# Kernel tuning notes

Hardware: AMD Instinct MI355X
Metric: run time of the kernel (lower is better)

## Reference

```python
import jax, jax.numpy as jnp
import numpy as np

N = 100000   # n_nodes
E = 600000   # n_edges
D = 128      # cfg_node_encoding_dim
L = 4        # nr_layers
EPS = 1e-5


def setup_inputs() -> dict:
    key = jax.random.key(0)
    k0, k1, k2, k3 = jax.random.split(key, 4)
    x = jax.random.normal(k0, (N, D), dtype=jnp.float32)
    edge_index = jax.random.randint(k1, (2, E), 0, N, dtype=jnp.int32)
    W = jax.random.normal(k2, (L, D, D), dtype=jnp.float32) * (1.0 / np.sqrt(D))
    b = jax.random.normal(k3, (L, D), dtype=jnp.float32) * 0.01
    gamma = jnp.ones((L, D), dtype=jnp.float32)
    beta = jnp.zeros((L, D), dtype=jnp.float32)
    return {"x": x, "W": W, "b": b, "gamma": gamma, "beta": beta,
            "edge_index": edge_index}


def _gcn_layer(x, W, b, src_sl, dst_sl, norm):
    # PyG GCNConv: h = x @ W, then symmetric-normalized aggregation + bias
    h = x @ W                                  # [N, D]
    msg = h[src_sl] * norm[:, None]            # [E+N, D] gather + scale
    out = jax.ops.segment_sum(msg, dst_sl, num_segments=N)  # scatter-add
    return out + b


def _layer_norm(x, gamma, beta):
    mu = jnp.mean(x, axis=-1, keepdims=True)
    var = jnp.mean(jnp.square(x - mu), axis=-1, keepdims=True)
    return (x - mu) * jax.lax.rsqrt(var + EPS) * gamma + beta


def reference(x, W, b, gamma, beta, edge_index):
    src, dst = edge_index[0], edge_index[1]
    loops = jnp.arange(N, dtype=edge_index.dtype)
    src_sl = jnp.concatenate([src, loops])     # add_self_loops=True
    dst_sl = jnp.concatenate([dst, loops])
    deg = jax.ops.segment_sum(jnp.ones(E + N, dtype=x.dtype), dst_sl,
                              num_segments=N)
    dinv = jnp.where(deg > 0, jax.lax.rsqrt(deg), 0.0)
    norm = dinv[src_sl] * dinv[dst_sl]         # D^{-1/2} (A+I) D^{-1/2}
    h = x
    for i in range(L):
        h = _gcn_layer(h, W[i], b[i], src_sl, dst_sl, norm)
        h = jax.nn.relu(h)
        # dropout is identity in eval mode
        h = _layer_norm(h, gamma[i], beta[i])
    return h
```

## Files before the change

kernel.cpp:

```cpp
#include <hip/hip_runtime.h>
#include <hip/hip_bf16.h>

#define D_DIM 128
#define AST 136

typedef __attribute__((ext_vector_type(8))) short short8v;
typedef __attribute__((ext_vector_type(4))) short short4v;
typedef __attribute__((ext_vector_type(4))) float floatx4;

__device__ __forceinline__ short f2bf(float x) {
    unsigned u = __builtin_bit_cast(unsigned, x);
    unsigned r = u + 0x7fff + ((u >> 16) & 1);
    return (short)(r >> 16);
}
__device__ __forceinline__ float bflo(unsigned p) {
    return __builtin_bit_cast(float, p << 16);
}
__device__ __forceinline__ float bfhi(unsigned p) {
    return __builtin_bit_cast(float, p & 0xffff0000u);
}


__global__ void zero_cnt_kernel(int* __restrict__ cnt, int n) {
    int i = blockIdx.x * blockDim.x + threadIdx.x;
    if (i < n) cnt[i] = 0;
}

__global__ void count_kernel(const int* __restrict__ dst, int* __restrict__ cnt, int e) {
    int i = blockIdx.x * blockDim.x + threadIdx.x;
    if (i < e) atomicAdd(&cnt[dst[i]], 1);
}

__global__ __launch_bounds__(256) void partial_kernel(const int* __restrict__ cnt,
                                                      int* __restrict__ partial, int n) {
    const int b = blockIdx.x, t = threadIdx.x;
    const int base = b * 1024 + t * 4;
    int s = 0;
    if (base + 3 < n) {
        int4 c = *(const int4*)(cnt + base);
        s = c.x + c.y + c.z + c.w;
    } else {
        for (int j = 0; j < 4; ++j) if (base + j < n) s += cnt[base + j];
    }
    #pragma unroll
    for (int m = 1; m < 64; m <<= 1) s += __shfl_xor(s, m, 64);
    __shared__ int ws[4];
    if ((t & 63) == 0) ws[t >> 6] = s;
    __syncthreads();
    if (t == 0) partial[b] = ws[0] + ws[1] + ws[2] + ws[3];
}

__global__ __launch_bounds__(1024) void scan_partials_kernel(int* __restrict__ partial, int nb,
                                                             int* __restrict__ row_ptr,
                                                             int n, int e) {
    __shared__ int sh[1024];
    const int t = threadIdx.x;
    sh[t] = (t < nb) ? partial[t] : 0;
    __syncthreads();
    for (int off = 1; off < 1024; off <<= 1) {
        int v = (t >= off) ? sh[t - off] : 0;
        __syncthreads();
        sh[t] += v;
        __syncthreads();
    }
    if (t < nb) partial[t] = (t == 0) ? 0 : sh[t - 1];
    if (t == 0) row_ptr[n] = e;
}

__global__ __launch_bounds__(256) void emit_kernel(const int* __restrict__ cnt,
                                                   const int* __restrict__ partial,
                                                   int* __restrict__ row_ptr,
                                                   int* __restrict__ cursor,
                                                   float* __restrict__ dinv, int n) {
    const int b = blockIdx.x, t = threadIdx.x;
    const int base = b * 1024 + t * 4;
    int4 c = make_int4(0, 0, 0, 0);
    if (base + 3 < n) {
        c = *(const int4*)(cnt + base);
    } else {
        if (base     < n) c.x = cnt[base];
        if (base + 1 < n) c.y = cnt[base + 1];
        if (base + 2 < n) c.z = cnt[base + 2];
        if (base + 3 < n) c.w = cnt[base + 3];
    }
    const int ts = c.x + c.y + c.z + c.w;
    int incl = ts;
    const int lane = t & 63;
    #pragma unroll
    for (int off = 1; off < 64; off <<= 1) {
        int v = __shfl_up(incl, off, 64);
        if (lane >= off) incl += v;
    }
    __shared__ int wsum[4];
    if (lane == 63) wsum[t >> 6] = incl;
    __syncthreads();
    const int w = t >> 6;
    int waveoff = 0;
    #pragma unroll
    for (int i = 0; i < 3; ++i) if (i < w) waveoff += wsum[i];
    const int basev = partial[b] + waveoff + (incl - ts);
    const int e0 = basev, e1 = e0 + c.x, e2 = e1 + c.y, e3 = e2 + c.z;
    if (base + 3 < n) {
        *(int4*)(row_ptr + base) = make_int4(e0, e1, e2, e3);
        *(int4*)(cursor  + base) = make_int4(e0, e1, e2, e3);
        *(float4*)(dinv + base) = make_float4(rsqrtf((float)(c.x + 1)), rsqrtf((float)(c.y + 1)),
                                              rsqrtf((float)(c.z + 1)), rsqrtf((float)(c.w + 1)));
    } else {
        int es[4] = {e0, e1, e2, e3};
        int cs[4] = {c.x, c.y, c.z, c.w};
        for (int j = 0; j < 4; ++j) if (base + j < n) {
            row_ptr[base + j] = es[j];
            cursor[base + j]  = es[j];
            dinv[base + j]    = rsqrtf((float)(cs[j] + 1));
        }
    }
}

__global__ void fill_kernel(const int* __restrict__ src, const int* __restrict__ dst,
                            const float* __restrict__ dinv,
                            int* __restrict__ cursor, int2* __restrict__ meta, int e) {
    int i = blockIdx.x * blockDim.x + threadIdx.x;
    if (i < e) {
        int s = src[i], d = dst[i];
        int p = atomicAdd(&cursor[d], 1);
        float w = dinv[s] * dinv[d];
        meta[p] = make_int2(s, __builtin_bit_cast(int, w));
    }
}

__global__ __launch_bounds__(256) void wt_prep_kernel(const float* __restrict__ W,
                                                      short* __restrict__ Wt, int total) {
    int o = blockIdx.x * blockDim.x + threadIdx.x;
    if (o >= total) return;
    int l = o >> 14;
    int r = o & 16383;
    int nn = r >> 7;
    int k  = r & 127;
    Wt[o] = f2bf(W[(size_t)l * 16384 + (size_t)k * 128 + nn]);
}

template <bool IN_F32>
__global__ __launch_bounds__(256) void gemm_mfma_kernel(const void* __restrict__ Xv,
                                                        const short* __restrict__ Wt,
                                                        short* __restrict__ H, int n) {
    __shared__ short Alds[64 * AST];
    const int t    = threadIdx.x;
    const int wv   = t >> 6;
    const int lane = t & 63;
    const int m    = lane & 15;
    const int quad = lane >> 4;
    const int row0 = blockIdx.x * 64;

    short8v bfr[2][4];
    #pragma unroll
    for (int c = 0; c < 2; ++c) {
        const short* bp = Wt + (size_t)((wv * 2 + c) * 16 + m) * D_DIM + quad * 8;
        #pragma unroll
        for (int kt = 0; kt < 4; ++kt)
            bfr[c][kt] = *(const short8v*)(bp + kt * 32);
    }

    if constexpr (IN_F32) {
        const float* X = (const float*)Xv;
        #pragma unroll
        for (int i = 0; i < 8; ++i) {
            int q  = t + i * 256;
            int r  = q >> 5;
            int k4 = q & 31;
            int row = row0 + r;
            float4 v = make_float4(0.f, 0.f, 0.f, 0.f);
            if (row < n) v = *(const float4*)(X + (size_t)row * D_DIM + k4 * 4);
            short4v s;
            s.x = f2bf(v.x); s.y = f2bf(v.y); s.z = f2bf(v.z); s.w = f2bf(v.w);
            *(short4v*)(&Alds[r * AST + k4 * 4]) = s;
        }
    } else {
        const short* X = (const short*)Xv;
        #pragma unroll
        for (int i = 0; i < 4; ++i) {
            int q  = t + i * 256;
            int r  = q >> 4;
            int kc = q & 15;
            int row = row0 + r;
            short8v v = {0,0,0,0,0,0,0,0};
            if (row < n) v = *(const short8v*)(X + (size_t)row * D_DIM + kc * 8);
            *(short8v*)(&Alds[r * AST + kc * 8]) = v;
        }
    }
    __syncthreads();

    #pragma unroll
    for (int rt = 0; rt < 4; ++rt) {
        const short* ab = &Alds[(rt * 16 + m) * AST + quad * 8];
        short8v afr[4];
        #pragma unroll
        for (int kt = 0; kt < 4; ++kt) afr[kt] = *(const short8v*)(ab + kt * 32);

        #pragma unroll
        for (int c = 0; c < 2; ++c) {
            floatx4 acc = (floatx4){0.f, 0.f, 0.f, 0.f};
            #pragma unroll
            for (int kt = 0; kt < 4; ++kt)
                acc = __builtin_amdgcn_mfma_f32_16x16x32_bf16(afr[kt], bfr[c][kt], acc, 0, 0, 0);
            const int col = (wv * 2 + c) * 16 + m;
            #pragma unroll
            for (int r = 0; r < 4; ++r) {
                const int row = row0 + rt * 16 + quad * 4 + r;
                if (row < n) H[(size_t)row * D_DIM + col] = f2bf(acc[r]);
            }
        }
    }
}

template <bool OUT_BF16>
__global__ __launch_bounds__(256) void agg_kernel(const short* __restrict__ Hb,
                                                  const int* __restrict__ row_ptr,
                                                  const int2* __restrict__ meta,
                                                  const float* __restrict__ dinv,
                                                  const float* __restrict__ bias,
                                                  const float* __restrict__ gamma,
                                                  const float* __restrict__ beta,
                                                  void* __restrict__ Yv, int n) {
    const int wave = __builtin_amdgcn_readfirstlane(threadIdx.x >> 6);
    const int lane = threadIdx.x & 63;
    const int v = blockIdx.x * 4 + wave;
    if (v >= n) return;

    const float dv = dinv[v];
    const int beg = row_ptr[v];
    const int end = row_ptr[v + 1];

    const unsigned ps = ((const unsigned*)(Hb + (size_t)v * D_DIM))[lane];
    const float wself = dv * dv;
    float ax = bflo(ps) * wself;
    float ay = bfhi(ps) * wself;

    for (int i = beg; i < end; i += 8) {
        int   idx[8];
        float wgt[8];
        #pragma unroll
        for (int j = 0; j < 8; ++j) {
            const int ii = min(i + j, end - 1);
            const int2 mm = meta[ii];
            idx[j] = mm.x;
            wgt[j] = (i + j < end) ? __builtin_bit_cast(float, mm.y) : 0.f;
        }
        unsigned p[8];
        #pragma unroll
        for (int j = 0; j < 8; ++j)
            p[j] = ((const unsigned*)(Hb + (size_t)idx[j] * D_DIM))[lane];
        #pragma unroll
        for (int j = 0; j < 8; ++j) {
            ax = fmaf(wgt[j], bflo(p[j]), ax);
            ay = fmaf(wgt[j], bfhi(p[j]), ay);
        }
    }

    const float2 bb = ((const float2*)bias)[lane];
    float a0 = fmaxf(ax + bb.x, 0.f);
    float a1 = fmaxf(ay + bb.y, 0.f);

    float s1 = a0 + a1;
    float s2 = a0 * a0 + a1 * a1;
    #pragma unroll
    for (int m = 1; m < 64; m <<= 1) {
        s1 += __shfl_xor(s1, m, 64);
        s2 += __shfl_xor(s2, m, 64);
    }
    const float mu  = s1 * (1.f / 128.f);
    const float var = s2 * (1.f / 128.f) - mu * mu;
    const float rs  = rsqrtf(var + 1e-5f);

    const float2 gg = ((const float2*)gamma)[lane];
    const float2 be = ((const float2*)beta)[lane];
    const float o0 = (a0 - mu) * rs * gg.x + be.x;
    const float o1 = (a1 - mu) * rs * gg.y + be.y;

    if constexpr (OUT_BF16) {
        unsigned pack = (unsigned)(unsigned short)f2bf(o0) |
                        ((unsigned)(unsigned short)f2bf(o1) << 16);
        ((unsigned*)((short*)Yv + (size_t)v * D_DIM))[lane] = pack;
    } else {
        float2 o; o.x = o0; o.y = o1;
        ((float2*)((float*)Yv + (size_t)v * D_DIM))[lane] = o;
    }
}


extern "C" void kernel_launch(void* const* d_in, const int* in_sizes, int n_in,
                              void* d_out, int out_size, void* d_ws, size_t ws_size,
                              hipStream_t stream) {
    const float* x     = (const float*)d_in[0];
    const float* W     = (const float*)d_in[1];
    const float* bias  = (const float*)d_in[2];
    const float* gamma = (const float*)d_in[3];
    const float* beta  = (const float*)d_in[4];
    const int*   edges = (const int*)d_in[5];

    const int N = in_sizes[0] / D_DIM;
    const int E = in_sizes[5] / 2;
    const int L = in_sizes[1] / (D_DIM * D_DIM);

    const int* src = edges;
    const int* dst = edges + E;

    const int NB = (N + 1023) / 1024;

    char* w = (char*)d_ws;
    short* Hb   = (short*)w; w += (size_t)N * D_DIM * sizeof(short);
    short* Act  = (short*)w; w += (size_t)N * D_DIM * sizeof(short);
    int* cnt     = (int*)w;  w += (size_t)((N + 3) & ~3) * sizeof(int);
    int* row_ptr = (int*)w;  w += (size_t)((N + 4) & ~3) * sizeof(int);
    int* cursor  = (int*)w;  w += (size_t)((N + 3) & ~3) * sizeof(int);
    int2* meta   = (int2*)w; w += (size_t)E * sizeof(int2);
    float* dinv  = (float*)w; w += (size_t)((N + 3) & ~3) * sizeof(float);
    int* partial = (int*)w;  w += (size_t)((NB + 3) & ~3) * sizeof(int);
    short* Wt    = (short*)w; w += (size_t)L * D_DIM * D_DIM * sizeof(short);

    zero_cnt_kernel<<<(N + 255) / 256, 256, 0, stream>>>(cnt, N);
    count_kernel<<<(E + 255) / 256, 256, 0, stream>>>(dst, cnt, E);
    partial_kernel<<<NB, 256, 0, stream>>>(cnt, partial, N);
    scan_partials_kernel<<<1, 1024, 0, stream>>>(partial, NB, row_ptr, N, E);
    emit_kernel<<<NB, 256, 0, stream>>>(cnt, partial, row_ptr, cursor, dinv, N);
    fill_kernel<<<(E + 255) / 256, 256, 0, stream>>>(src, dst, dinv, cursor, meta, E);

    const int WT_TOTAL = L * D_DIM * D_DIM;
    wt_prep_kernel<<<(WT_TOTAL + 255) / 256, 256, 0, stream>>>(W, Wt, WT_TOTAL);

    const int GB = (N + 63) / 64;
    const int AB = (N + 3) / 4;

    gemm_mfma_kernel<true><<<GB, 256, 0, stream>>>(x, Wt, Hb, N);
    agg_kernel<true><<<AB, 256, 0, stream>>>(Hb, row_ptr, meta, dinv,
                                             bias, gamma, beta, Act, N);
    for (int l = 1; l < L - 1; ++l) {
        gemm_mfma_kernel<false><<<GB, 256, 0, stream>>>(Act, Wt + (size_t)l * D_DIM * D_DIM, Hb, N);
        agg_kernel<true><<<AB, 256, 0, stream>>>(Hb, row_ptr, meta, dinv,
                                                 bias + (size_t)l * D_DIM,
                                                 gamma + (size_t)l * D_DIM,
                                                 beta + (size_t)l * D_DIM, Act, N);
    }
    {
        int l = L - 1;
        gemm_mfma_kernel<false><<<GB, 256, 0, stream>>>(Act, Wt + (size_t)l * D_DIM * D_DIM, Hb, N);
        agg_kernel<false><<<AB, 256, 0, stream>>>(Hb, row_ptr, meta, dinv,
                                                  bias + (size_t)l * D_DIM,
                                                  gamma + (size_t)l * D_DIM,
                                                  beta + (size_t)l * D_DIM, d_out, N);
    }
}
```

Before: 381.8 us.

## Fuse aggregation, GEMM, bias, ReLU and LayerNorm into one per-layer kernel

Reorders each GCN layer to aggregate first and transform second, (A·X)·W instead of A·(X·W). Each block of 64 rows gathers the normalized neighbor sum into LDS as bf16, runs the MFMA GEMM, and applies bias, ReLU and LayerNorm in-register, using LDS atomics for the row statistics. This removes the separate GEMM output buffer and its round trip through global memory, and halves the launches per layer. In exchange, the first layer gathers fp32 input rows, outputs are written as per-column scalar stores, and the aggregation runs serially over 16 rows per wave inside the block.

```diff
diff --git a/kernel.cpp b/kernel.cpp
--- a/kernel.cpp
+++ b/kernel.cpp
@@ -139,11 +139,21 @@
     Wt[o] = f2bf(W[(size_t)l * 16384 + (size_t)k * 128 + nn]);
 }
 
-template <bool IN_F32>
-__global__ __launch_bounds__(256) void gemm_mfma_kernel(const void* __restrict__ Xv,
-                                                        const short* __restrict__ Wt,
-                                                        short* __restrict__ H, int n) {
+template <bool IN_F32, bool OUT_F32>
+__global__ __launch_bounds__(256, 4) void fused_layer_kernel(const void* __restrict__ Xv,
+                                                             const short* __restrict__ Wt,
+                                                             const int* __restrict__ row_ptr,
+                                                             const int2* __restrict__ meta,
+                                                             const float* __restrict__ dinv,
+                                                             const float* __restrict__ bias,
+                                                             const float* __restrict__ gamma,
+                                                             const float* __restrict__ beta,
+                                                             void* __restrict__ Yv, int n) {
     __shared__ short Alds[64 * AST];
+    __shared__ float Ps1[64 * 17];
+    __shared__ float Ps2[64 * 17];
+    __shared__ float2 MuRs[64];
+
     const int t    = threadIdx.x;
     const int wv   = t >> 6;
     const int lane = t & 63;
@@ -151,6 +161,8 @@
     const int quad = lane >> 4;
     const int row0 = blockIdx.x * 64;
 
+    for (int i = t; i < 64 * 17; i += 256) { Ps1[i] = 0.f; Ps2[i] = 0.f; }
+
     short8v bfr[2][4];
     #pragma unroll
     for (int c = 0; c < 2; ++c) {
@@ -160,129 +172,137 @@
             bfr[c][kt] = *(const short8v*)(bp + kt * 32);
     }
 
-    if constexpr (IN_F32) {
-        const float* X = (const float*)Xv;
-        #pragma unroll
-        for (int i = 0; i < 8; ++i) {
-            int q  = t + i * 256;
-            int r  = q >> 5;
-            int k4 = q & 31;
-            int row = row0 + r;
-            float4 v = make_float4(0.f, 0.f, 0.f, 0.f);
-            if (row < n) v = *(const float4*)(X + (size_t)row * D_DIM + k4 * 4);
-            short4v s;
-            s.x = f2bf(v.x); s.y = f2bf(v.y); s.z = f2bf(v.z); s.w = f2bf(v.w);
-            *(short4v*)(&Alds[r * AST + k4 * 4]) = s;
-        }
-    } else {
-        const short* X = (const short*)Xv;
-        #pragma unroll
-        for (int i = 0; i < 4; ++i) {
-            int q  = t + i * 256;
-            int r  = q >> 4;
-            int kc = q & 15;
-            int row = row0 + r;
-            short8v v = {0,0,0,0,0,0,0,0};
-            if (row < n) v = *(const short8v*)(X + (size_t)row * D_DIM + kc * 8);
-            *(short8v*)(&Alds[r * AST + kc * 8]) = v;
-        }
-    }
-    __syncthreads();
-
+    for (int rr = 0; rr < 16; ++rr) {
+        const int v = row0 + wv * 16 + rr;
+        float ax = 0.f, ay = 0.f;
+        if (v < n) {
+            const float dv = dinv[v];
+            const int beg = row_ptr[v];
+            const int end = row_ptr[v + 1];
+            const float wself = dv * dv;
+            if constexpr (IN_F32) {
+                const float2 p = ((const float2*)((const float*)Xv + (size_t)v * D_DIM))[lane];
+                ax = p.x * wself; ay = p.y * wself;
+            } else {
+                const unsigned p = ((const unsigned*)((const short*)Xv + (size_t)v * D_DIM))[lane];
+                ax = bflo(p) * wself; ay = bfhi(p) * wself;
+            }
+            for (int i = beg; i < end; i += 8) {
+                int   idx[8];
+                float wgt[8];
+                #pragma unroll
+                for (int j = 0; j < 8; ++j) {
+                    const int ii = min(i + j, end - 1);
+                    const int2 mm = meta[ii];
+                    idx[j] = mm.x;
+                    wgt[j] = (i + j < end) ? __builtin_bit_cast(float, mm.y) : 0.f;
+                }
+                if constexpr (IN_F32) {
+                    float2 p[8];
+                    #pragma unroll
+                    for (int j = 0; j < 8; ++j)
+                        p[j] = ((const float2*)((const float*)Xv + (size_t)idx[j] * D_DIM))[lane];
+                    #pragma unroll
+                    for (int j = 0; j < 8; ++j) {
+                        ax = fmaf(wgt[j], p[j].x, ax);
+                        ay = fmaf(wgt[j], p[j].y, ay);
+                    }
+                } else {
+                    unsigned p[8];
+                    #pragma unroll
+                    for (int j = 0; j < 8; ++j)
+                        p[j] = ((const unsigned*)((const short*)Xv + (size_t)idx[j] * D_DIM))[lane];
+                    #pragma unroll
+                    for (int j = 0; j < 8; ++j) {
+                        ax = fmaf(wgt[j], bflo(p[j]), ax);
+                        ay = fmaf(wgt[j], bfhi(p[j]), ay);
+                    }
+                }
+            }
+        }
+        const unsigned pk = (unsigned)(unsigned short)f2bf(ax) |
+                            ((unsigned)(unsigned short)f2bf(ay) << 16);
+        *(unsigned*)&Alds[(wv * 16 + rr) * AST + lane * 2] = pk;
+    }
+    __syncthreads();
+
+    floatx4 acc[4][2];
     #pragma unroll
     for (int rt = 0; rt < 4; ++rt) {
         const short* ab = &Alds[(rt * 16 + m) * AST + quad * 8];
         short8v afr[4];
         #pragma unroll
         for (int kt = 0; kt < 4; ++kt) afr[kt] = *(const short8v*)(ab + kt * 32);
-
         #pragma unroll
         for (int c = 0; c < 2; ++c) {
-            floatx4 acc = (floatx4){0.f, 0.f, 0.f, 0.f};
+            floatx4 a = (floatx4){0.f, 0.f, 0.f, 0.f};
             #pragma unroll
             for (int kt = 0; kt < 4; ++kt)
-                acc = __builtin_amdgcn_mfma_f32_16x16x32_bf16(afr[kt], bfr[c][kt], acc, 0, 0, 0);
-            const int col = (wv * 2 + c) * 16 + m;
-            #pragma unroll
-            for (int r = 0; r < 4; ++r) {
-                const int row = row0 + rt * 16 + quad * 4 + r;
-                if (row < n) H[(size_t)row * D_DIM + col] = f2bf(acc[r]);
+                a = __builtin_amdgcn_mfma_f32_16x16x32_bf16(afr[kt], bfr[c][kt], a, 0, 0, 0);
+            acc[rt][c] = a;
+        }
+    }
+
+    const int col0 = wv * 32 + m;
+    const int col1 = col0 + 16;
+    const float b0 = bias[col0], b1 = bias[col1];
+    #pragma unroll
+    for (int rt = 0; rt < 4; ++rt) {
+        #pragma unroll
+        for (int r = 0; r < 4; ++r) {
+            const float v0 = fmaxf(acc[rt][0][r] + b0, 0.f);
+            const float v1 = fmaxf(acc[rt][1][r] + b1, 0.f);
+            acc[rt][0][r] = v0;
+            acc[rt][1][r] = v1;
+            const int row = rt * 16 + quad * 4 + r;
+            atomicAdd(&Ps1[row * 17 + m], v0 + v1);
+            atomicAdd(&Ps2[row * 17 + m], v0 * v0 + v1 * v1);
+        }
+    }
+    __syncthreads();
+
+    {
+        const int row = t >> 2;
+        const int g = t & 3;
+        float s1 = 0.f, s2 = 0.f;
+        #pragma unroll
+        for (int j = 0; j < 4; ++j) {
+            s1 += Ps1[row * 17 + g * 4 + j];
+            s2 += Ps2[row * 17 + g * 4 + j];
+        }
+        s1 += __shfl_xor(s1, 1, 64);  s2 += __shfl_xor(s2, 1, 64);
+        s1 += __shfl_xor(s1, 2, 64);  s2 += __shfl_xor(s2, 2, 64);
+        if (g == 0) {
+            const float mu  = s1 * (1.f / 128.f);
+            const float var = s2 * (1.f / 128.f) - mu * mu;
+            MuRs[row] = make_float2(mu, rsqrtf(var + 1e-5f));
+        }
+    }
+    __syncthreads();
+
+    const float g0  = gamma[col0], g1  = gamma[col1];
+    const float be0 = beta[col0],  be1 = beta[col1];
+    #pragma unroll
+    for (int rt = 0; rt < 4; ++rt) {
+        #pragma unroll
+        for (int r = 0; r < 4; ++r) {
+            const int row  = rt * 16 + quad * 4 + r;
+            const int grow = row0 + row;
+            if (grow < n) {
+                const float2 ms = MuRs[row];
+                const float o0 = (acc[rt][0][r] - ms.x) * ms.y * g0 + be0;
+                const float o1 = (acc[rt][1][r] - ms.x) * ms.y * g1 + be1;
+                if constexpr (OUT_F32) {
+                    float* Y = (float*)Yv + (size_t)grow * D_DIM;
+                    Y[col0] = o0;
+                    Y[col1] = o1;
+                } else {
+                    short* Y = (short*)Yv + (size_t)grow * D_DIM;
+                    Y[col0] = f2bf(o0);
+                    Y[col1] = f2bf(o1);
+                }
             }
         }
-    }
-}
-
-template <bool OUT_BF16>
-__global__ __launch_bounds__(256) void agg_kernel(const short* __restrict__ Hb,
-                                                  const int* __restrict__ row_ptr,
-                                                  const int2* __restrict__ meta,
-                                                  const float* __restrict__ dinv,
-                                                  const float* __restrict__ bias,
-                                                  const float* __restrict__ gamma,
-                                                  const float* __restrict__ beta,
-                                                  void* __restrict__ Yv, int n) {
-    const int wave = __builtin_amdgcn_readfirstlane(threadIdx.x >> 6);
-    const int lane = threadIdx.x & 63;
-    const int v = blockIdx.x * 4 + wave;
-    if (v >= n) return;
-
-    const float dv = dinv[v];
-    const int beg = row_ptr[v];
-    const int end = row_ptr[v + 1];
-
-    const unsigned ps = ((const unsigned*)(Hb + (size_t)v * D_DIM))[lane];
-    const float wself = dv * dv;
-    float ax = bflo(ps) * wself;
-    float ay = bfhi(ps) * wself;
-
-    for (int i = beg; i < end; i += 8) {
-        int   idx[8];
-        float wgt[8];
-        #pragma unroll
-        for (int j = 0; j < 8; ++j) {
-            const int ii = min(i + j, end - 1);
-            const int2 mm = meta[ii];
-            idx[j] = mm.x;
-            wgt[j] = (i + j < end) ? __builtin_bit_cast(float, mm.y) : 0.f;
-        }
-        unsigned p[8];
-        #pragma unroll
-        for (int j = 0; j < 8; ++j)
-            p[j] = ((const unsigned*)(Hb + (size_t)idx[j] * D_DIM))[lane];
-        #pragma unroll
-        for (int j = 0; j < 8; ++j) {
-            ax = fmaf(wgt[j], bflo(p[j]), ax);
-            ay = fmaf(wgt[j], bfhi(p[j]), ay);
-        }
-    }
-
-    const float2 bb = ((const float2*)bias)[lane];
-    float a0 = fmaxf(ax + bb.x, 0.f);
-    float a1 = fmaxf(ay + bb.y, 0.f);
-
-    float s1 = a0 + a1;
-    float s2 = a0 * a0 + a1 * a1;
-    #pragma unroll
-    for (int m = 1; m < 64; m <<= 1) {
-        s1 += __shfl_xor(s1, m, 64);
-        s2 += __shfl_xor(s2, m, 64);
-    }
-    const float mu  = s1 * (1.f / 128.f);
-    const float var = s2 * (1.f / 128.f) - mu * mu;
-    const float rs  = rsqrtf(var + 1e-5f);
-
-    const float2 gg = ((const float2*)gamma)[lane];
-    const float2 be = ((const float2*)beta)[lane];
-    const float o0 = (a0 - mu) * rs * gg.x + be.x;
-    const float o1 = (a1 - mu) * rs * gg.y + be.y;
-
-    if constexpr (OUT_BF16) {
-        unsigned pack = (unsigned)(unsigned short)f2bf(o0) |
-                        ((unsigned)(unsigned short)f2bf(o1) << 16);
-        ((unsigned*)((short*)Yv + (size_t)v * D_DIM))[lane] = pack;
-    } else {
-        float2 o; o.x = o0; o.y = o1;
-        ((float2*)((float*)Yv + (size_t)v * D_DIM))[lane] = o;
     }
 }
 
@@ -307,8 +327,8 @@
     const int NB = (N + 1023) / 1024;
 
     char* w = (char*)d_ws;
-    short* Hb   = (short*)w; w += (size_t)N * D_DIM * sizeof(short);
-    short* Act  = (short*)w; w += (size_t)N * D_DIM * sizeof(short);
+    short* ActA = (short*)w; w += (size_t)N * D_DIM * sizeof(short);
+    short* ActB = (short*)w; w += (size_t)N * D_DIM * sizeof(short);
     int* cnt     = (int*)w;  w += (size_t)((N + 3) & ~3) * sizeof(int);
     int* row_ptr = (int*)w;  w += (size_t)((N + 4) & ~3) * sizeof(int);
     int* cursor  = (int*)w;  w += (size_t)((N + 3) & ~3) * sizeof(int);
@@ -328,24 +348,31 @@
     wt_prep_kernel<<<(WT_TOTAL + 255) / 256, 256, 0, stream>>>(W, Wt, WT_TOTAL);
 
     const int GB = (N + 63) / 64;
-    const int AB = (N + 3) / 4;
-
-    gemm_mfma_kernel<true><<<GB, 256, 0, stream>>>(x, Wt, Hb, N);
-    agg_kernel<true><<<AB, 256, 0, stream>>>(Hb, row_ptr, meta, dinv,
-                                             bias, gamma, beta, Act, N);
+
+    if (L == 1) {
+        fused_layer_kernel<true, true><<<GB, 256, 0, stream>>>(x, Wt, row_ptr, meta, dinv,
+                                                               bias, gamma, beta, d_out, N);
+        return;
+    }
+
+    fused_layer_kernel<true, false><<<GB, 256, 0, stream>>>(x, Wt, row_ptr, meta, dinv,
+                                                            bias, gamma, beta, ActA, N);
+    const short* cur = ActA;
     for (int l = 1; l < L - 1; ++l) {
-        gemm_mfma_kernel<false><<<GB, 256, 0, stream>>>(Act, Wt + (size_t)l * D_DIM * D_DIM, Hb, N);
-        agg_kernel<true><<<AB, 256, 0, stream>>>(Hb, row_ptr, meta, dinv,
-                                                 bias + (size_t)l * D_DIM,
-                                                 gamma + (size_t)l * D_DIM,
-                                                 beta + (size_t)l * D_DIM, Act, N);
+        short* nxt = (l & 1) ? ActB : ActA;
+        fused_layer_kernel<false, false><<<GB, 256, 0, stream>>>(cur, Wt + (size_t)l * D_DIM * D_DIM,
+                                                                 row_ptr, meta, dinv,
+                                                                 bias + (size_t)l * D_DIM,
+                                                                 gamma + (size_t)l * D_DIM,
+                                                                 beta + (size_t)l * D_DIM, nxt, N);
+        cur = nxt;
     }
     {
-        int l = L - 1;
-        gemm_mfma_kernel<false><<<GB, 256, 0, stream>>>(Act, Wt + (size_t)l * D_DIM * D_DIM, Hb, N);
-        agg_kernel<false><<<AB, 256, 0, stream>>>(Hb, row_ptr, meta, dinv,
-                                                  bias + (size_t)l * D_DIM,
-                                                  gamma + (size_t)l * D_DIM,
-                                                  beta + (size_t)l * D_DIM, d_out, N);
-    }
-}
+        const int l = L - 1;
+        fused_layer_kernel<false, true><<<GB, 256, 0, stream>>>(cur, Wt + (size_t)l * D_DIM * D_DIM,
+                                                                row_ptr, meta, dinv,
+                                                                bias + (size_t)l * D_DIM,
+                                                                gamma + (size_t)l * D_DIM,
+                                                                beta + (size_t)l * D_DIM, d_out, N);
+    }
+}
```

After: 718.3 us. 88.1% more time.

## Stage GEMM output through LDS and aggregate two nodes per wave

Applied to the files above, without the earlier changes.

The GEMM epilogue now writes the bf16 results into shared memory and then stores full 16-byte row chunks to global memory, replacing scattered 2-byte stores. The aggregation kernel now processes two destination nodes per wave, interleaving four neighbours from each so that eight gathers stay in flight while fewer padded lanes are wasted on low-degree nodes. In exchange, the GEMM gains extra barriers and LDS traffic, and nodes with unequal degree leave some lanes idle until the larger neighbour count is covered.

```diff
diff --git a/kernel.cpp b/kernel.cpp
--- a/kernel.cpp
+++ b/kernel.cpp
@@ -3,6 +3,7 @@
 
 #define D_DIM 128
 #define AST 136
+#define CST 132
 
 typedef __attribute__((ext_vector_type(8))) short short8v;
 typedef __attribute__((ext_vector_type(4))) short short4v;
@@ -189,6 +190,7 @@
     }
     __syncthreads();
 
+    floatx4 acc[4][2];
     #pragma unroll
     for (int rt = 0; rt < 4; ++rt) {
         const short* ab = &Alds[(rt * 16 + m) * AST + quad * 8];
@@ -198,17 +200,35 @@
 
         #pragma unroll
         for (int c = 0; c < 2; ++c) {
-            floatx4 acc = (floatx4){0.f, 0.f, 0.f, 0.f};
+            floatx4 a = (floatx4){0.f, 0.f, 0.f, 0.f};
             #pragma unroll
             for (int kt = 0; kt < 4; ++kt)
-                acc = __builtin_amdgcn_mfma_f32_16x16x32_bf16(afr[kt], bfr[c][kt], acc, 0, 0, 0);
+                a = __builtin_amdgcn_mfma_f32_16x16x32_bf16(afr[kt], bfr[c][kt], a, 0, 0, 0);
+            acc[rt][c] = a;
+        }
+    }
+    __syncthreads();
+
+    #pragma unroll
+    for (int rt = 0; rt < 4; ++rt) {
+        #pragma unroll
+        for (int c = 0; c < 2; ++c) {
             const int col = (wv * 2 + c) * 16 + m;
             #pragma unroll
-            for (int r = 0; r < 4; ++r) {
-                const int row = row0 + rt * 16 + quad * 4 + r;
-                if (row < n) H[(size_t)row * D_DIM + col] = f2bf(acc[r]);
-            }
-        }
+            for (int r = 0; r < 4; ++r)
+                Alds[(rt * 16 + quad * 4 + r) * CST + col] = f2bf(acc[rt][c][r]);
+        }
+    }
+    __syncthreads();
+
+    #pragma unroll
+    for (int i = 0; i < 4; ++i) {
+        int q  = t + i * 256;
+        int r  = q >> 4;
+        int kc = q & 15;
+        int row = row0 + r;
+        if (row < n)
+            *(short8v*)(H + (size_t)row * D_DIM + kc * 8) = *(const short8v*)(&Alds[r * CST + kc * 8]);
     }
 }
 
@@ -223,66 +243,88 @@
                                                   void* __restrict__ Yv, int n) {
     const int wave = __builtin_amdgcn_readfirstlane(threadIdx.x >> 6);
     const int lane = threadIdx.x & 63;
-    const int v = blockIdx.x * 4 + wave;
-    if (v >= n) return;
-
-    const float dv = dinv[v];
-    const int beg = row_ptr[v];
-    const int end = row_ptr[v + 1];
-
-    const unsigned ps = ((const unsigned*)(Hb + (size_t)v * D_DIM))[lane];
-    const float wself = dv * dv;
-    float ax = bflo(ps) * wself;
-    float ay = bfhi(ps) * wself;
-
-    for (int i = beg; i < end; i += 8) {
+    const int vA = (blockIdx.x * 4 + wave) * 2;
+    if (vA >= n) return;
+    const bool hasB = (vA + 1) < n;
+    const int vB = hasB ? vA + 1 : vA;
+
+    const float dvA = dinv[vA];
+    const float dvB = dinv[vB];
+    const int begA = row_ptr[vA];
+    const int endA = row_ptr[vA + 1];
+    const int begB = row_ptr[vB];
+    const int endB = row_ptr[vB + 1];
+    const int cntA = endA - begA;
+    const int cntB = hasB ? (endB - begB) : 0;
+    const int mx = cntA > cntB ? cntA : cntB;
+
+    const unsigned psA = ((const unsigned*)(Hb + (size_t)vA * D_DIM))[lane];
+    const unsigned psB = ((const unsigned*)(Hb + (size_t)vB * D_DIM))[lane];
+    float axA = bflo(psA) * (dvA * dvA);
+    float ayA = bfhi(psA) * (dvA * dvA);
+    float axB = bflo(psB) * (dvB * dvB);
+    float ayB = bfhi(psB) * (dvB * dvB);
+
+    for (int k = 0; k < mx; k += 4) {
         int   idx[8];
         float wgt[8];
         #pragma unroll
-        for (int j = 0; j < 8; ++j) {
-            const int ii = min(i + j, end - 1);
+        for (int j = 0; j < 4; ++j) {
+            int ii = min(begA + k + j, endA - 1); ii = max(ii, 0);
             const int2 mm = meta[ii];
             idx[j] = mm.x;
-            wgt[j] = (i + j < end) ? __builtin_bit_cast(float, mm.y) : 0.f;
+            wgt[j] = (k + j < cntA) ? __builtin_bit_cast(float, mm.y) : 0.f;
+        }
+        #pragma unroll
+        for (int j = 0; j < 4; ++j) {
+            int ii = min(begB + k + j, endB - 1); ii = max(ii, 0);
+            const int2 mm = meta[ii];
+            idx[4 + j] = mm.x;
+            wgt[4 + j] = (k + j < cntB) ? __builtin_bit_cast(float, mm.y) : 0.f;
         }
         unsigned p[8];
         #pragma unroll
         for (int j = 0; j < 8; ++j)
             p[j] = ((const unsigned*)(Hb + (size_t)idx[j] * D_DIM))[lane];
         #pragma unroll
-        for (int j = 0; j < 8; ++j) {
-            ax = fmaf(wgt[j], bflo(p[j]), ax);
-            ay = fmaf(wgt[j], bfhi(p[j]), ay);
+        for (int j = 0; j < 4; ++j) {
+            axA = fmaf(wgt[j], bflo(p[j]), axA);
+            ayA = fmaf(wgt[j], bfhi(p[j]), ayA);
+            axB = fmaf(wgt[4 + j], bflo(p[4 + j]), axB);
+            ayB = fmaf(wgt[4 + j], bfhi(p[4 + j]), ayB);
         }
     }
 
     const float2 bb = ((const float2*)bias)[lane];
-    float a0 = fmaxf(ax + bb.x, 0.f);
-    float a1 = fmaxf(ay + bb.y, 0.f);
-
-    float s1 = a0 + a1;
-    float s2 = a0 * a0 + a1 * a1;
-    #pragma unroll
-    for (int m = 1; m < 64; m <<= 1) {
-        s1 += __shfl_xor(s1, m, 64);
-        s2 += __shfl_xor(s2, m, 64);
-    }
-    const float mu  = s1 * (1.f / 128.f);
-    const float var = s2 * (1.f / 128.f) - mu * mu;
-    const float rs  = rsqrtf(var + 1e-5f);
-
     const float2 gg = ((const float2*)gamma)[lane];
     const float2 be = ((const float2*)beta)[lane];
-    const float o0 = (a0 - mu) * rs * gg.x + be.x;
-    const float o1 = (a1 - mu) * rs * gg.y + be.y;
-
-    if constexpr (OUT_BF16) {
-        unsigned pack = (unsigned)(unsigned short)f2bf(o0) |
-                        ((unsigned)(unsigned short)f2bf(o1) << 16);
-        ((unsigned*)((short*)Yv + (size_t)v * D_DIM))[lane] = pack;
-    } else {
-        float2 o; o.x = o0; o.y = o1;
-        ((float2*)((float*)Yv + (size_t)v * D_DIM))[lane] = o;
+
+    #pragma unroll
+    for (int s = 0; s < 2; ++s) {
+        if (s == 1 && !hasB) break;
+        float a0 = fmaxf((s ? axB : axA) + bb.x, 0.f);
+        float a1 = fmaxf((s ? ayB : ayA) + bb.y, 0.f);
+        float s1 = a0 + a1;
+        float s2 = a0 * a0 + a1 * a1;
+        #pragma unroll
+        for (int m = 1; m < 64; m <<= 1) {
+            s1 += __shfl_xor(s1, m, 64);
+            s2 += __shfl_xor(s2, m, 64);
+        }
+        const float mu  = s1 * (1.f / 128.f);
+        const float var = s2 * (1.f / 128.f) - mu * mu;
+        const float rs  = rsqrtf(var + 1e-5f);
+        const float o0 = (a0 - mu) * rs * gg.x + be.x;
+        const float o1 = (a1 - mu) * rs * gg.y + be.y;
+        const int v = s ? vB : vA;
+        if constexpr (OUT_BF16) {
+            unsigned pack = (unsigned)(unsigned short)f2bf(o0) |
+                            ((unsigned)(unsigned short)f2bf(o1) << 16);
+            ((unsigned*)((short*)Yv + (size_t)v * D_DIM))[lane] = pack;
+        } else {
+            float2 o; o.x = o0; o.y = o1;
+            ((float2*)((float*)Yv + (size_t)v * D_DIM))[lane] = o;
+        }
     }
 }
 
@@ -328,7 +370,7 @@
     wt_prep_kernel<<<(WT_TOTAL + 255) / 256, 256, 0, stream>>>(W, Wt, WT_TOTAL);
 
     const int GB = (N + 63) / 64;
-    const int AB = (N + 3) / 4;
+    const int AB = (N + 7) / 8;
 
     gemm_mfma_kernel<true><<<GB, 256, 0, stream>>>(x, Wt, Hb, N);
     agg_kernel<true><<<AB, 256, 0, stream>>>(Hb, row_ptr, meta, dinv,
```

Result: faster. 367.6 us (-3.7%).
